# Optimization experiments

Measured on AMD Instinct MI355X. Metric: run time of the kernel, lower is better.

## Reference

```python
import jax, jax.numpy as jnp
import numpy as np
import math

D_MODEL = 1024
N_HEADS = 16
SPARSITY = 0.3


def setup_inputs() -> dict:
    key = jax.random.key(0)
    ks = jax.random.split(key, 12)
    B, S, D = 4, 2048, D_MODEL
    Dh = D // 2
    sc = 0.02
    inp = {
        "x": jax.random.normal(ks[0], (B, S, D), dtype=jnp.float32),
        "wq": jax.random.normal(ks[1], (D, D), dtype=jnp.float32) * sc,
        "bq": jnp.zeros((D,), jnp.float32),
        "wk": jax.random.normal(ks[2], (D, D), dtype=jnp.float32) * sc,
        "bk": jnp.zeros((D,), jnp.float32),
        "wv": jax.random.normal(ks[3], (D, D), dtype=jnp.float32) * sc,
        "bv": jnp.zeros((D,), jnp.float32),
        "wo": jax.random.normal(ks[4], (D, D), dtype=jnp.float32) * sc,
        "bo": jnp.zeros((D,), jnp.float32),
        "wi1": jax.random.normal(ks[5], (Dh, D), dtype=jnp.float32) * sc,
        "bi1": jnp.zeros((Dh,), jnp.float32),
        "wi2": jax.random.normal(ks[6], (1, Dh), dtype=jnp.float32) * sc,
        "bi2": jnp.zeros((1,), jnp.float32),
    }
    return inp


def reference(x, wq, bq, wk, bk, wv, bv, wo, bo, wi1, bi1, wi2, bi2):
    B, S, D = x.shape
    H = N_HEADS
    hd = D // H
    k = max(1, int(S * SPARSITY))

    # projections (torch Linear: x @ W^T + b)
    Q = (x @ wq.T + bq).reshape(B, S, H, hd).transpose(0, 2, 1, 3)  # [B,H,S,hd]
    K = (x @ wk.T + bk).reshape(B, S, H, hd).transpose(0, 2, 1, 3)
    V = (x @ wv.T + bv).reshape(B, S, H, hd).transpose(0, 2, 1, 3)

    # learned indexer -> per-position importance [B,S]
    h = jnp.maximum(x @ wi1.T + bi1, 0.0)
    importance = (h @ wi2.T + bi2)[..., 0]

    _, top_idx = jax.lax.top_k(importance, k)  # [B,k]
    sparse_mask = jnp.zeros((B, S), dtype=x.dtype).at[
        jnp.arange(B)[:, None], top_idx
    ].set(1.0)

    scores = jnp.einsum("bhqd,bhkd->bhqk", Q, K) / math.sqrt(hd)
    scores = jnp.where(sparse_mask[:, None, None, :] == 0, -jnp.inf, scores)
    attn = jax.nn.softmax(scores, axis=-1)

    out = jnp.einsum("bhqk,bhkd->bhqd", attn, V)
    out = out.transpose(0, 2, 1, 3).reshape(B, S, D)
    return out @ wo.T + bo
```

## Files before the change

kernel.cpp:

```cpp
#include <hip/hip_runtime.h>
#include <math.h>

#define BB 4
#define SS 2048
#define DD 1024
#define HHD 16
#define HD 64
#define DH 512
#define KSEL 614
#define KPAD 640
#define MTOT (BB*SS)
#define NCH (KPAD/64)
#define MKV (BB*KPAD)

typedef __attribute__((ext_vector_type(8))) short bf16x8;
typedef __attribute__((ext_vector_type(4))) float f32x4;

#define LDS_CAST(p) ((__attribute__((address_space(3))) void*)(p))
#define GLB_CAST(p) ((const __attribute__((address_space(1))) void*)(p))

#define QK_SCALE 0.18033688011112042f

__device__ inline short bf16rne(float v)
{
    unsigned u = __builtin_bit_cast(unsigned, v);
    return (short)((u + 0x7FFFu + ((u >> 16) & 1u)) >> 16);
}

__device__ inline void split1(float v, short& h, short& l)
{
    unsigned u = __builtin_bit_cast(unsigned, v);
    unsigned hr = (u + 0x7FFFu + ((u >> 16) & 1u)) >> 16;
    h = (short)hr;
    float hf = __builtin_bit_cast(float, hr << 16);
    float res = v - hf;
    unsigned u2 = __builtin_bit_cast(unsigned, res);
    unsigned lr = (u2 + 0x7FFFu + ((u2 >> 16) & 1u)) >> 16;
    l = (short)lr;
}

__global__ __launch_bounds__(256)
void split_convert(const float* __restrict__ in, short* __restrict__ hi,
                   short* __restrict__ lo, int n4)
{
    const int i = blockIdx.x * 256 + threadIdx.x;
    if (i >= n4) return;
    float4 v = reinterpret_cast<const float4*>(in)[i];
    short4 h, l;
    split1(v.x, h.x, l.x);
    split1(v.y, h.y, l.y);
    split1(v.z, h.z, l.z);
    split1(v.w, h.w, l.w);
    reinterpret_cast<short4*>(hi)[i] = h;
    reinterpret_cast<short4*>(lo)[i] = l;
}

__global__ __launch_bounds__(256)
void split_weights(const float* __restrict__ wq, const float* __restrict__ wk,
                   const float* __restrict__ wv, const float* __restrict__ wo,
                   const float* __restrict__ wi1,
                   const float* __restrict__ bk, const float* __restrict__ bv,
                   short* __restrict__ Bqkv_hi, short* __restrict__ wo_hi,
                   short* __restrict__ Wi_hi, short* __restrict__ Wi_lo,
                   float* __restrict__ bkv)
{
    const int i = blockIdx.x * 256 + threadIdx.x;
    const int which = blockIdx.y;
    if (which < 4) {
        const float* src = (which == 0) ? wq : (which == 1) ? wk : (which == 2) ? wv : wo;
        short* dst = (which == 3) ? wo_hi : (Bqkv_hi + (size_t)which * DD * DD);
        float4 v = reinterpret_cast<const float4*>(src)[i];
        short4 hh;
        hh.x = bf16rne(v.x); hh.y = bf16rne(v.y); hh.z = bf16rne(v.z); hh.w = bf16rne(v.w);
        reinterpret_cast<short4*>(dst)[i] = hh;
    } else if (which == 4) {
        if (i >= DH*DD/4) return;
        float4 v = reinterpret_cast<const float4*>(wi1)[i];
        short4 h, l;
        split1(v.x, h.x, l.x); split1(v.y, h.y, l.y);
        split1(v.z, h.z, l.z); split1(v.w, h.w, l.w);
        reinterpret_cast<short4*>(Wi_hi)[i] = h;
        reinterpret_cast<short4*>(Wi_lo)[i] = l;
    } else {
        if (i >= 2048) return;
        bkv[i] = (i < 1024) ? bk[i] : bv[i - 1024];
    }
}

template<bool BF16_OUT, bool QSCALE>
__global__ __launch_bounds__(256)
void gemm_bf16(const short* __restrict__ Ahi, const short* __restrict__ Bhi,
               const float* __restrict__ bias, void* __restrict__ Cv,
               int M, int N, int K, int ldc)
{
    __shared__ short sAh[128*64];
    __shared__ short sBh[128*64];

    const int t = threadIdx.x;
    const int lane = t & 63, wid = t >> 6;
    const int wm = wid >> 1, wn = wid & 1;
    const int row0 = blockIdx.y * 128, col0 = blockIdx.x * 128;
    const int g = lane >> 4, r = lane & 15;
    const int lrow = lane >> 3;
    const int lslot = lane & 7;

    f32x4 acc[4][4];
    #pragma unroll
    for (int mt = 0; mt < 4; ++mt)
        #pragma unroll
        for (int nt = 0; nt < 4; ++nt) acc[mt][nt] = (f32x4){0.f, 0.f, 0.f, 0.f};

    for (int k0 = 0; k0 < K; k0 += 64) {
        #pragma unroll
        for (int e = 0; e < 4; ++e) {
            const int rl = wid * 32 + e * 8 + lrow;
            const int scol = k0 + ((lslot ^ (rl & 7)) << 3);
            const size_t ga = (size_t)(row0 + rl) * K + scol;
            const size_t gb = (size_t)(col0 + rl) * K + scol;
            const int ldso = (wid * 32 + e * 8) * 64;
            __builtin_amdgcn_global_load_lds(GLB_CAST(Ahi + ga), LDS_CAST(sAh + ldso), 16, 0, 0);
            __builtin_amdgcn_global_load_lds(GLB_CAST(Bhi + gb), LDS_CAST(sBh + ldso), 16, 0, 0);
        }
        __syncthreads();

        #pragma unroll
        for (int kk = 0; kk < 2; ++kk) {
            bf16x8 ah[4], bh[4];
            #pragma unroll
            for (int mt = 0; mt < 4; ++mt) {
                const int rw = wm * 64 + mt * 16 + r;
                ah[mt] = *reinterpret_cast<const bf16x8*>(sAh + rw * 64 + (((kk*4 + g) ^ (rw & 7)) << 3));
            }
            #pragma unroll
            for (int nt = 0; nt < 4; ++nt) {
                const int rw = wn * 64 + nt * 16 + r;
                bh[nt] = *reinterpret_cast<const bf16x8*>(sBh + rw * 64 + (((kk*4 + g) ^ (rw & 7)) << 3));
            }
            #pragma unroll
            for (int mt = 0; mt < 4; ++mt)
                #pragma unroll
                for (int nt = 0; nt < 4; ++nt)
                    acc[mt][nt] = __builtin_amdgcn_mfma_f32_16x16x32_bf16(ah[mt], bh[nt], acc[mt][nt], 0, 0, 0);
        }
        __syncthreads();
    }

    #pragma unroll
    for (int nt = 0; nt < 4; ++nt) {
        const int col = wn * 64 + nt * 16 + r;
        const float bv = bias[col0 + col];
        const bool qs = QSCALE && (col0 + col) < 1024;
        #pragma unroll
        for (int mt = 0; mt < 4; ++mt) {
            #pragma unroll
            for (int e = 0; e < 4; ++e) {
                const int row = row0 + wm * 64 + mt * 16 + 4 * g + e;
                float v = acc[mt][nt][e] + bv;
                if (qs) v *= QK_SCALE;
                if (BF16_OUT)
                    ((short*)Cv)[(size_t)row * ldc + col0 + col] = bf16rne(v);
                else
                    ((float*)Cv)[(size_t)row * ldc + col0 + col] = v;
            }
        }
    }
}

__global__ __launch_bounds__(256)
void idx_q_fused(const short* __restrict__ x_hi, const short* __restrict__ x_lo,
                 const short* __restrict__ Wq_hi, const float* __restrict__ bq,
                 short* __restrict__ Qb,
                 const short* __restrict__ Wi_hi, const short* __restrict__ Wi_lo,
                 const float* __restrict__ bi1, float* __restrict__ Hw)
{
    __shared__ __align__(16) char smem[32768];
    const int t = threadIdx.x;
    const int lane = t & 63, wid = t >> 6;
    const int g = lane >> 4, r = lane & 15;

    if ((blockIdx.x & 1) == 0) {
        const int id = blockIdx.x >> 1;
        const int row0 = (id >> 3) * 128, col0 = (id & 7) * 128;
        short* sAh = (short*)smem;
        short* sBh = sAh + 128*64;
        const int wm = wid >> 1, wn = wid & 1;
        const int lrow = lane >> 3;
        const int lslot = lane & 7;

        f32x4 acc[4][4];
        #pragma unroll
        for (int mt = 0; mt < 4; ++mt)
            #pragma unroll
            for (int nt = 0; nt < 4; ++nt) acc[mt][nt] = (f32x4){0.f, 0.f, 0.f, 0.f};

        for (int k0 = 0; k0 < DD; k0 += 64) {
            #pragma unroll
            for (int e = 0; e < 4; ++e) {
                const int rl = wid * 32 + e * 8 + lrow;
                const int scol = k0 + ((lslot ^ (rl & 7)) << 3);
                const size_t ga = (size_t)(row0 + rl) * DD + scol;
                const size_t gb = (size_t)(col0 + rl) * DD + scol;
                const int ldso = (wid * 32 + e * 8) * 64;
                __builtin_amdgcn_global_load_lds(GLB_CAST(x_hi + ga), LDS_CAST(sAh + ldso), 16, 0, 0);
                __builtin_amdgcn_global_load_lds(GLB_CAST(Wq_hi + gb), LDS_CAST(sBh + ldso), 16, 0, 0);
            }
            __syncthreads();

            #pragma unroll
            for (int kk = 0; kk < 2; ++kk) {
                bf16x8 ah[4], bh[4];
                #pragma unroll
                for (int mt = 0; mt < 4; ++mt) {
                    const int rw = wm * 64 + mt * 16 + r;
                    ah[mt] = *reinterpret_cast<const bf16x8*>(sAh + rw * 64 + (((kk*4 + g) ^ (rw & 7)) << 3));
                }
                #pragma unroll
                for (int nt = 0; nt < 4; ++nt) {
                    const int rw = wn * 64 + nt * 16 + r;
                    bh[nt] = *reinterpret_cast<const bf16x8*>(sBh + rw * 64 + (((kk*4 + g) ^ (rw & 7)) << 3));
                }
                #pragma unroll
                for (int mt = 0; mt < 4; ++mt)
                    #pragma unroll
                    for (int nt = 0; nt < 4; ++nt)
                        acc[mt][nt] = __builtin_amdgcn_mfma_f32_16x16x32_bf16(ah[mt], bh[nt], acc[mt][nt], 0, 0, 0);
            }
            __syncthreads();
        }

        #pragma unroll
        for (int nt = 0; nt < 4; ++nt) {
            const int col = wn * 64 + nt * 16 + r;
            const float bv = bq[col0 + col];
            #pragma unroll
            for (int mt = 0; mt < 4; ++mt) {
                #pragma unroll
                for (int e = 0; e < 4; ++e) {
                    const int row = row0 + wm * 64 + mt * 16 + 4 * g + e;
                    Qb[(size_t)row * DD + col0 + col] = bf16rne((acc[mt][nt][e] + bv) * QK_SCALE);
                }
            }
        }
    } else {
        const int id = blockIdx.x >> 1;
        const int row0 = (id >> 2) * 64, col0 = (id & 3) * 128;
        short* sAh = (short*)smem;
        short* sAl = sAh + 64*32;
        short* sBh = sAl + 64*32;
        short* sBl = sBh + 128*32;
        const int srow = lane >> 2;
        const int sslot = lane & 3;

        f32x4 acc[4][2];
        #pragma unroll
        for (int mt = 0; mt < 4; ++mt)
            #pragma unroll
            for (int nt = 0; nt < 2; ++nt) acc[mt][nt] = (f32x4){0.f, 0.f, 0.f, 0.f};

        for (int k0 = 0; k0 < DD; k0 += 32) {
            {
                const int rl = wid * 16 + srow;
                const int scol = k0 + ((sslot ^ ((rl >> 2) & 3)) << 3);
                const size_t ga = (size_t)(row0 + rl) * DD + scol;
                const int ldso = (wid * 16) * 32;
                __builtin_amdgcn_global_load_lds(GLB_CAST(x_hi + ga), LDS_CAST(sAh + ldso), 16, 0, 0);
                __builtin_amdgcn_global_load_lds(GLB_CAST(x_lo + ga), LDS_CAST(sAl + ldso), 16, 0, 0);
            }
            #pragma unroll
            for (int i = 0; i < 2; ++i) {
                const int rl = i * 64 + wid * 16 + srow;
                const int scol = k0 + ((sslot ^ ((rl >> 2) & 3)) << 3);
                const size_t gb = (size_t)(col0 + rl) * DD + scol;
                const int ldso = (i * 64 + wid * 16) * 32;
                __builtin_amdgcn_global_load_lds(GLB_CAST(Wi_hi + gb), LDS_CAST(sBh + ldso), 16, 0, 0);
                __builtin_amdgcn_global_load_lds(GLB_CAST(Wi_lo + gb), LDS_CAST(sBl + ldso), 16, 0, 0);
            }
            __syncthreads();

            bf16x8 ah[4], al[4], bh[2], bl[2];
            #pragma unroll
            for (int mt = 0; mt < 4; ++mt) {
                const int row = mt * 16 + r;
                const int sw = g ^ ((row >> 2) & 3);
                ah[mt] = *reinterpret_cast<const bf16x8*>(sAh + row * 32 + sw * 8);
                al[mt] = *reinterpret_cast<const bf16x8*>(sAl + row * 32 + sw * 8);
            }
            #pragma unroll
            for (int nt = 0; nt < 2; ++nt) {
                const int row = wid * 32 + nt * 16 + r;
                const int sw = g ^ ((row >> 2) & 3);
                bh[nt] = *reinterpret_cast<const bf16x8*>(sBh + row * 32 + sw * 8);
                bl[nt] = *reinterpret_cast<const bf16x8*>(sBl + row * 32 + sw * 8);
            }
            #pragma unroll
            for (int mt = 0; mt < 4; ++mt)
                #pragma unroll
                for (int nt = 0; nt < 2; ++nt) {
                    acc[mt][nt] = __builtin_amdgcn_mfma_f32_16x16x32_bf16(ah[mt], bh[nt], acc[mt][nt], 0, 0, 0);
                    acc[mt][nt] = __builtin_amdgcn_mfma_f32_16x16x32_bf16(ah[mt], bl[nt], acc[mt][nt], 0, 0, 0);
                    acc[mt][nt] = __builtin_amdgcn_mfma_f32_16x16x32_bf16(al[mt], bh[nt], acc[mt][nt], 0, 0, 0);
                }
            __syncthreads();
        }

        #pragma unroll
        for (int nt = 0; nt < 2; ++nt) {
            const int col = wid * 32 + nt * 16 + r;
            const float bv = bi1[col0 + col];
            #pragma unroll
            for (int mt = 0; mt < 4; ++mt) {
                #pragma unroll
                for (int e = 0; e < 4; ++e) {
                    const int row = row0 + mt * 16 + 4 * g + e;
                    Hw[(size_t)row * DH + col0 + col] = fmaxf(acc[mt][nt][e] + bv, 0.f);
                }
            }
        }
    }
}

__global__ __launch_bounds__(256)
void gemm_kv_gather(const short* __restrict__ Ahi, const short* __restrict__ Bhi,
                    const int* __restrict__ idxg, const float* __restrict__ bias,
                    short* __restrict__ C)
{
    __shared__ short sAh[128*64];
    __shared__ short sBh[128*64];

    const int K = DD, N = 2048;
    const int t = threadIdx.x;
    const int lane = t & 63, wid = t >> 6;
    const int wm = wid >> 1, wn = wid & 1;
    const int row0 = blockIdx.y * 128, col0 = blockIdx.x * 128;
    const int g = lane >> 4, r = lane & 15;
    const int lrow = lane >> 3;
    const int lslot = lane & 7;

    size_t garow[4];
    #pragma unroll
    for (int e = 0; e < 4; ++e) {
        const int rl = row0 + wid * 32 + e * 8 + lrow;
        const int grow = (rl / KPAD) * SS + idxg[rl];
        garow[e] = (size_t)grow * K;
    }

    f32x4 acc[4][4];
    #pragma unroll
    for (int mt = 0; mt < 4; ++mt)
        #pragma unroll
        for (int nt = 0; nt < 4; ++nt) acc[mt][nt] = (f32x4){0.f, 0.f, 0.f, 0.f};

    for (int k0 = 0; k0 < K; k0 += 64) {
        #pragma unroll
        for (int e = 0; e < 4; ++e) {
            const int rl = wid * 32 + e * 8 + lrow;
            const int scol = k0 + ((lslot ^ (rl & 7)) << 3);
            const size_t gb = (size_t)(col0 + rl) * K + scol;
            const int ldso = (wid * 32 + e * 8) * 64;
            __builtin_amdgcn_global_load_lds(GLB_CAST(Ahi + garow[e] + scol), LDS_CAST(sAh + ldso), 16, 0, 0);
            __builtin_amdgcn_global_load_lds(GLB_CAST(Bhi + gb), LDS_CAST(sBh + ldso), 16, 0, 0);
        }
        __syncthreads();

        #pragma unroll
        for (int kk = 0; kk < 2; ++kk) {
            bf16x8 ah[4], bh[4];
            #pragma unroll
            for (int mt = 0; mt < 4; ++mt) {
                const int rw = wm * 64 + mt * 16 + r;
                ah[mt] = *reinterpret_cast<const bf16x8*>(sAh + rw * 64 + (((kk*4 + g) ^ (rw & 7)) << 3));
            }
            #pragma unroll
            for (int nt = 0; nt < 4; ++nt) {
                const int rw = wn * 64 + nt * 16 + r;
                bh[nt] = *reinterpret_cast<const bf16x8*>(sBh + rw * 64 + (((kk*4 + g) ^ (rw & 7)) << 3));
            }
            #pragma unroll
            for (int mt = 0; mt < 4; ++mt)
                #pragma unroll
                for (int nt = 0; nt < 4; ++nt)
                    acc[mt][nt] = __builtin_amdgcn_mfma_f32_16x16x32_bf16(ah[mt], bh[nt], acc[mt][nt], 0, 0, 0);
        }
        __syncthreads();
    }

    #pragma unroll
    for (int nt = 0; nt < 4; ++nt) {
        const int col = wn * 64 + nt * 16 + r;
        const float bv = bias[col0 + col];
        #pragma unroll
        for (int mt = 0; mt < 4; ++mt) {
            #pragma unroll
            for (int e = 0; e < 4; ++e) {
                const int row = row0 + wm * 64 + mt * 16 + 4 * g + e;
                C[(size_t)row * N + col0 + col] = bf16rne(acc[mt][nt][e] + bv);
            }
        }
    }
}

__global__ __launch_bounds__(256)
void importance_kernel(const float* __restrict__ h, const float* __restrict__ wi2,
                       const float* __restrict__ bi2, float* __restrict__ imp)
{
    const int wid = threadIdx.x >> 6, lane = threadIdx.x & 63;
    const int row = blockIdx.x * 4 + wid;
    const float* hr = h + (size_t)row * DH;
    float s = 0.f;
    #pragma unroll
    for (int i = 0; i < DH/64; ++i)
        s = fmaf(hr[lane + i*64], wi2[lane + i*64], s);
    #pragma unroll
    for (int off = 32; off; off >>= 1) s += __shfl_down(s, off);
    if (lane == 0) imp[row] = s + bi2[0];
}

__global__ __launch_bounds__(256)
void rank_kernel(const float* __restrict__ imp, int* __restrict__ flags)
{
    __shared__ float simp[SS];
    const int b = blockIdx.y;
    const int t = threadIdx.x;
    const float* bimp = imp + b * SS;
    for (int i = t; i < SS/4; i += 256)
        reinterpret_cast<float4*>(simp)[i] = reinterpret_cast<const float4*>(bimp)[i];
    __syncthreads();

    const int i = blockIdx.x * 32 + (t >> 3);
    const int part = t & 7;
    const float v = simp[i];
    const float4* slice = reinterpret_cast<const float4*>(simp + part * (SS/8));
    const int jb = part * (SS/8);
    int rank = 0;
    #pragma unroll 8
    for (int jj = 0; jj < SS/32; ++jj) {
        const float4 u4 = slice[jj];
        const int j = jb + jj * 4;
        rank += (u4.x > v) || ((u4.x == v) && (j + 0 < i));
        rank += (u4.y > v) || ((u4.y == v) && (j + 1 < i));
        rank += (u4.z > v) || ((u4.z == v) && (j + 2 < i));
        rank += (u4.w > v) || ((u4.w == v) && (j + 3 < i));
    }
    rank += __shfl_xor(rank, 1);
    rank += __shfl_xor(rank, 2);
    rank += __shfl_xor(rank, 4);
    if (part == 0) flags[b * SS + i] = (rank < KSEL) ? 1 : 0;
}

__global__ __launch_bounds__(256)
void compact_kernel(const int* __restrict__ flags, int* __restrict__ idxg)
{
    __shared__ int sscan[SS];
    __shared__ int sidx[KSEL];
    const int b = blockIdx.x, t = threadIdx.x;
    for (int i = t; i < SS; i += 256) sscan[i] = flags[b * SS + i];
    __syncthreads();
    for (int off = 1; off < SS; off <<= 1) {
        int vals[SS/256];
        #pragma unroll
        for (int c = 0; c < SS/256; ++c) {
            const int i = t + c * 256;
            int v = sscan[i];
            if (i >= off) v += sscan[i - off];
            vals[c] = v;
        }
        __syncthreads();
        #pragma unroll
        for (int c = 0; c < SS/256; ++c) sscan[t + c * 256] = vals[c];
        __syncthreads();
    }
    for (int i = t; i < SS; i += 256) {
        const int f = flags[b * SS + i];
        if (f) sidx[sscan[i] - 1] = i;
    }
    __syncthreads();
    for (int p = t; p < KPAD; p += 256)
        idxg[b * KPAD + p] = sidx[min(p, KSEL - 1)];
}

__global__ __launch_bounds__(256)
void gather_kv(const short* __restrict__ KVc, short* __restrict__ Kg,
               short* __restrict__ Vg)
{
    __shared__ short Vs[64*72];
    const int t = threadIdx.x;
    const int c = blockIdx.x, h = blockIdx.y, b = blockIdx.z;
    const int srow = t >> 2;
    const int sq4  = t & 3;

    const size_t cbase = ((size_t)(b * HHD + h) * NCH + c) * 4096;

    const short* kb = KVc + (size_t)(b * KPAD + c * 64 + srow) * 2048 + h * HD + sq4 * 16;
    bf16x8 k0 = *reinterpret_cast<const bf16x8*>(kb);
    bf16x8 k1 = *reinterpret_cast<const bf16x8*>(kb + 8);
    short* kout = Kg + cbase + srow * HD + sq4 * 16;
    *reinterpret_cast<bf16x8*>(kout)     = k0;
    *reinterpret_cast<bf16x8*>(kout + 8) = k1;

    const short* vbp = kb + 1024;
    bf16x8 v0 = *reinterpret_cast<const bf16x8*>(vbp);
    bf16x8 v1 = *reinterpret_cast<const bf16x8*>(vbp + 8);
    #pragma unroll
    for (int j = 0; j < 8; ++j) {
        Vs[(sq4 * 16 + j) * 72 + srow]     = v0[j];
        Vs[(sq4 * 16 + 8 + j) * 72 + srow] = v1[j];
    }
    __syncthreads();

    const int x = 8 * (srow >> 4);
    short* vout = Vg + cbase + srow * 64;
    *reinterpret_cast<bf16x8*>(vout + ((sq4 * 16)     ^ x)) = *reinterpret_cast<const bf16x8*>(&Vs[srow * 72 + sq4 * 16]);
    *reinterpret_cast<bf16x8*>(vout + ((sq4 * 16 + 8) ^ x)) = *reinterpret_cast<const bf16x8*>(&Vs[srow * 72 + sq4 * 16 + 8]);
}

__global__ __launch_bounds__(512)
void attn_mfma(const short* __restrict__ Qb, const short* __restrict__ Kg,
               const short* __restrict__ Vg, short* __restrict__ AOhi)
{
    __shared__ short Ks[2][64*72];
    __shared__ short Vs[2][64*72];
    __shared__ short Ps[8][16*72];

    const int t = threadIdx.x;
    const int lane = t & 63, w = t >> 6;
    const int g = lane >> 4, r = lane & 15;
    const int qt = blockIdx.x, h = blockIdx.y, b = blockIdx.z;
    const int q0 = qt * 128;
    short* Psw = &Ps[w][0];

    const int srow = t >> 3;
    const int scol = (t & 7) * 8;
    const short* kcbase = Kg + ((size_t)(b * HHD + h) * NCH) * 4096 + srow * 64 + scol;
    const short* vcbase = Vg + ((size_t)(b * HHD + h) * NCH) * 4096 + srow * 64 + scol;

    bf16x8 qh[2];
    {
        const short* qrow = Qb + (size_t)(b * SS + q0 + w * 16 + r) * DD + h * HD;
        qh[0] = *reinterpret_cast<const bf16x8*>(qrow + 8 * g);
        qh[1] = *reinterpret_cast<const bf16x8*>(qrow + 32 + 8 * g);
    }

    bf16x8 ones;
    #pragma unroll
    for (int j = 0; j < 8; ++j) ones[j] = (short)0x3F80;

    f32x4 oacc[4];
    #pragma unroll
    for (int dt = 0; dt < 4; ++dt) oacc[dt] = (f32x4){0.f, 0.f, 0.f, 0.f};
    f32x4 dacc = (f32x4){0.f, 0.f, 0.f, 0.f};

    bf16x8 kreg = *reinterpret_cast<const bf16x8*>(kcbase);
    bf16x8 vreg = *reinterpret_cast<const bf16x8*>(vcbase);

    for (int c = 0; c < NCH; ++c) {
        const int cur = c & 1;
        *reinterpret_cast<bf16x8*>(&Ks[cur][srow*72 + scol]) = kreg;
        *reinterpret_cast<bf16x8*>(&Vs[cur][srow*72 + scol]) = vreg;
        if (c + 1 < NCH) {
            kreg = *reinterpret_cast<const bf16x8*>(kcbase + (size_t)(c + 1) * 4096);
            vreg = *reinterpret_cast<const bf16x8*>(vcbase + (size_t)(c + 1) * 4096);
        }
        __syncthreads();

        f32x4 sa[4];
        #pragma unroll
        for (int kt = 0; kt < 4; ++kt) {
            bf16x8 kf0 = *reinterpret_cast<const bf16x8*>(&Ks[cur][(kt*16 + r)*72 + 8*g]);
            bf16x8 kf1 = *reinterpret_cast<const bf16x8*>(&Ks[cur][(kt*16 + r)*72 + 32 + 8*g]);
            f32x4 s = (f32x4){0.f, 0.f, 0.f, 0.f};
            s = __builtin_amdgcn_mfma_f32_16x16x32_bf16(qh[0], kf0, s, 0, 0, 0);
            s = __builtin_amdgcn_mfma_f32_16x16x32_bf16(qh[1], kf1, s, 0, 0, 0);
            sa[kt] = s;
        }
        if (c == NCH - 1) {
            #pragma unroll
            for (int kt = 0; kt < 4; ++kt)
                if (c*64 + kt*16 + r >= KSEL)
                    sa[kt] = (f32x4){-INFINITY, -INFINITY, -INFINITY, -INFINITY};
        }

        #pragma unroll
        for (int kt = 0; kt < 4; ++kt)
            #pragma unroll
            for (int e = 0; e < 4; ++e)
                Psw[(4*g + e)*72 + ((kt*16 + r) ^ (8*g))] =
                    (short)(__builtin_bit_cast(unsigned, exp2f(sa[kt][e])) >> 16);

        #pragma unroll
        for (int kc = 0; kc < 2; ++kc) {
            bf16x8 pf = *reinterpret_cast<const bf16x8*>(&Psw[r*72 + kc*32 + 8*(g ^ (r >> 2))]);
            dacc = __builtin_amdgcn_mfma_f32_16x16x32_bf16(pf, ones, dacc, 0, 0, 0);
            #pragma unroll
            for (int dt = 0; dt < 4; ++dt) {
                bf16x8 vf = *reinterpret_cast<const bf16x8*>(&Vs[cur][(dt*16 + r)*72 + kc*32 + 8*(g ^ dt)]);
                oacc[dt] = __builtin_amdgcn_mfma_f32_16x16x32_bf16(pf, vf, oacc[dt], 0, 0, 0);
            }
        }
    }

    #pragma unroll
    for (int dt = 0; dt < 4; ++dt)
        #pragma unroll
        for (int e = 0; e < 4; ++e) {
            const size_t a = (size_t)(b * SS + q0 + w*16 + 4*g + e) * DD + h * HD + dt*16 + r;
            AOhi[a] = bf16rne(oacc[dt][e] / dacc[e]);
        }
}

extern "C" void kernel_launch(void* const* d_in, const int* in_sizes, int n_in,
                              void* d_out, int out_size, void* d_ws, size_t ws_size,
                              hipStream_t stream)
{
    const float* x   = (const float*)d_in[0];
    const float* wq  = (const float*)d_in[1];
    const float* bq  = (const float*)d_in[2];
    const float* wk  = (const float*)d_in[3];
    const float* bk  = (const float*)d_in[4];
    const float* wv  = (const float*)d_in[5];
    const float* bv  = (const float*)d_in[6];
    const float* wo  = (const float*)d_in[7];
    const float* bo  = (const float*)d_in[8];
    const float* wi1 = (const float*)d_in[9];
    const float* bi1 = (const float*)d_in[10];
    const float* wi2 = (const float*)d_in[11];
    const float* bi2 = (const float*)d_in[12];
    float* out = (float*)d_out;

    const size_t MB = 1ull << 20;
    char* W = (char*)d_ws;
    short* x_hi  = (short*)(W + 0);
    short* x_lo  = (short*)(W + 16*MB);
    short* Qb    = (short*)(W + 32*MB);
    short* KVc   = (short*)(W + 48*MB);
    short* Wi_hi = (short*)(W + 96*MB);
    short* Wi_lo = (short*)(W + 97*MB);
    short* Bqkv_hi=(short*)(W + 128*MB);
    short* wo_hi = (short*)(W + 134*MB);
    float* Hw    = (float*)(W + 144*MB);
    short* Kg    = (short*)(W + 144*MB);
    short* Vg    = (short*)(W + 150*MB);
    float* bkv   = (float*)(W + 160*MB);
    float* imp   = (float*)(W + 160*MB + 64*1024);
    int*   flags = (int*)(W + 160*MB + 128*1024);
    int*   idxg  = (int*)(W + 160*MB + 192*1024);
    short* AO_hi = x_hi;

    const size_t NM = (size_t)MTOT * DD;

    split_convert<<<(NM/4 + 255)/256, 256, 0, stream>>>(x, x_hi, x_lo, NM/4);
    split_weights<<<dim3(DD*DD/4/256, 6), 256, 0, stream>>>(
        wq, wk, wv, wo, wi1, bk, bv, Bqkv_hi, wo_hi, Wi_hi, Wi_lo, bkv);

    idx_q_fused<<<1024, 256, 0, stream>>>(
        x_hi, x_lo, Bqkv_hi, bq, Qb, Wi_hi, Wi_lo, bi1, Hw);

    importance_kernel<<<MTOT/4, 256, 0, stream>>>(Hw, wi2, bi2, imp);
    rank_kernel<<<dim3(SS/32, BB), 256, 0, stream>>>(imp, flags);
    compact_kernel<<<BB, 256, 0, stream>>>(flags, idxg);

    gemm_kv_gather<<<dim3(2048/128, MKV/128), 256, 0, stream>>>(
        x_hi, Bqkv_hi + (size_t)DD*DD, idxg, bkv, KVc);

    gather_kv<<<dim3(NCH, HHD, BB), 256, 0, stream>>>(KVc, Kg, Vg);

    attn_mfma<<<dim3(SS/128, HHD, BB), 512, 0, stream>>>(Qb, Kg, Vg, AO_hi);

    gemm_bf16<false, false><<<dim3(DD/128, MTOT/128), 256, 0, stream>>>(
        AO_hi, wo_hi, bo, out, MTOT, DD, DD, DD);
}
```

Baseline: 200.4 us.

## Fuse Q and gathered KV projections into one kernel, scatter KV directly

```diff
diff --git a/kernel.cpp b/kernel.cpp
--- a/kernel.cpp
+++ b/kernel.cpp
@@ -87,10 +87,9 @@
     }
 }
 
-template<bool BF16_OUT, bool QSCALE>
 __global__ __launch_bounds__(256)
 void gemm_bf16(const short* __restrict__ Ahi, const short* __restrict__ Bhi,
-               const float* __restrict__ bias, void* __restrict__ Cv,
+               const float* __restrict__ bias, float* __restrict__ C,
                int M, int N, int K, int ldc)
 {
     __shared__ short sAh[128*64];
@@ -149,49 +148,43 @@
     for (int nt = 0; nt < 4; ++nt) {
         const int col = wn * 64 + nt * 16 + r;
         const float bv = bias[col0 + col];
-        const bool qs = QSCALE && (col0 + col) < 1024;
         #pragma unroll
         for (int mt = 0; mt < 4; ++mt) {
             #pragma unroll
             for (int e = 0; e < 4; ++e) {
                 const int row = row0 + wm * 64 + mt * 16 + 4 * g + e;
-                float v = acc[mt][nt][e] + bv;
-                if (qs) v *= QK_SCALE;
-                if (BF16_OUT)
-                    ((short*)Cv)[(size_t)row * ldc + col0 + col] = bf16rne(v);
-                else
-                    ((float*)Cv)[(size_t)row * ldc + col0 + col] = v;
-            }
-        }
-    }
-}
-
-__global__ __launch_bounds__(256)
-void idx_q_fused(const short* __restrict__ x_hi, const short* __restrict__ x_lo,
-                 const short* __restrict__ Wq_hi, const float* __restrict__ bq,
-                 short* __restrict__ Qb,
-                 const short* __restrict__ Wi_hi, const short* __restrict__ Wi_lo,
-                 const float* __restrict__ bi1, float* __restrict__ Hw)
+                C[(size_t)row * ldc + col0 + col] = acc[mt][nt][e] + bv;
+            }
+        }
+    }
+}
+
+__global__ __launch_bounds__(256)
+void qkv_fused(const short* __restrict__ x_hi, const short* __restrict__ Bqkv_hi,
+               const float* __restrict__ bq, const float* __restrict__ bkv,
+               const int* __restrict__ idxg,
+               short* __restrict__ Qb, short* __restrict__ Kg, short* __restrict__ Vg)
 {
     __shared__ __align__(16) char smem[32768];
+    short* sAh = (short*)smem;
+    short* sBh = sAh + 128*64;
+
     const int t = threadIdx.x;
     const int lane = t & 63, wid = t >> 6;
+    const int wm = wid >> 1, wn = wid & 1;
     const int g = lane >> 4, r = lane & 15;
-
-    if ((blockIdx.x & 1) == 0) {
-        const int id = blockIdx.x >> 1;
+    const int lrow = lane >> 3;
+    const int lslot = lane & 7;
+
+    f32x4 acc[4][4];
+    #pragma unroll
+    for (int mt = 0; mt < 4; ++mt)
+        #pragma unroll
+        for (int nt = 0; nt < 4; ++nt) acc[mt][nt] = (f32x4){0.f, 0.f, 0.f, 0.f};
+
+    if (blockIdx.x < 512) {
+        const int id = blockIdx.x;
         const int row0 = (id >> 3) * 128, col0 = (id & 7) * 128;
-        short* sAh = (short*)smem;
-        short* sBh = sAh + 128*64;
-        const int wm = wid >> 1, wn = wid & 1;
-        const int lrow = lane >> 3;
-        const int lslot = lane & 7;
-
-        f32x4 acc[4][4];
-        #pragma unroll
-        for (int mt = 0; mt < 4; ++mt)
-            #pragma unroll
-            for (int nt = 0; nt < 4; ++nt) acc[mt][nt] = (f32x4){0.f, 0.f, 0.f, 0.f};
 
         for (int k0 = 0; k0 < DD; k0 += 64) {
             #pragma unroll
@@ -202,7 +195,7 @@
                 const size_t gb = (size_t)(col0 + rl) * DD + scol;
                 const int ldso = (wid * 32 + e * 8) * 64;
                 __builtin_amdgcn_global_load_lds(GLB_CAST(x_hi + ga), LDS_CAST(sAh + ldso), 16, 0, 0);
-                __builtin_amdgcn_global_load_lds(GLB_CAST(Wq_hi + gb), LDS_CAST(sBh + ldso), 16, 0, 0);
+                __builtin_amdgcn_global_load_lds(GLB_CAST(Bqkv_hi + gb), LDS_CAST(sBh + ldso), 16, 0, 0);
             }
             __syncthreads();
 
@@ -242,158 +235,163 @@
             }
         }
     } else {
-        const int id = blockIdx.x >> 1;
-        const int row0 = (id >> 2) * 64, col0 = (id & 3) * 128;
-        short* sAh = (short*)smem;
-        short* sAl = sAh + 64*32;
-        short* sBh = sAl + 64*32;
-        short* sBl = sBh + 128*32;
-        const int srow = lane >> 2;
-        const int sslot = lane & 3;
-
-        f32x4 acc[4][2];
-        #pragma unroll
-        for (int mt = 0; mt < 4; ++mt)
-            #pragma unroll
-            for (int nt = 0; nt < 2; ++nt) acc[mt][nt] = (f32x4){0.f, 0.f, 0.f, 0.f};
-
-        for (int k0 = 0; k0 < DD; k0 += 32) {
-            {
-                const int rl = wid * 16 + srow;
-                const int scol = k0 + ((sslot ^ ((rl >> 2) & 3)) << 3);
-                const size_t ga = (size_t)(row0 + rl) * DD + scol;
-                const int ldso = (wid * 16) * 32;
-                __builtin_amdgcn_global_load_lds(GLB_CAST(x_hi + ga), LDS_CAST(sAh + ldso), 16, 0, 0);
-                __builtin_amdgcn_global_load_lds(GLB_CAST(x_lo + ga), LDS_CAST(sAl + ldso), 16, 0, 0);
-            }
-            #pragma unroll
-            for (int i = 0; i < 2; ++i) {
-                const int rl = i * 64 + wid * 16 + srow;
-                const int scol = k0 + ((sslot ^ ((rl >> 2) & 3)) << 3);
+        const int id = blockIdx.x - 512;
+        const int row0 = (id >> 4) * 128;
+        const int col0 = (id & 15) * 128;
+        const short* Bw = Bqkv_hi + (size_t)DD * DD;
+
+        size_t garow[4];
+        #pragma unroll
+        for (int e = 0; e < 4; ++e) {
+            const int rl = row0 + wid * 32 + e * 8 + lrow;
+            const int grow = (rl / KPAD) * SS + idxg[rl];
+            garow[e] = (size_t)grow * DD;
+        }
+
+        for (int k0 = 0; k0 < DD; k0 += 64) {
+            #pragma unroll
+            for (int e = 0; e < 4; ++e) {
+                const int rl = wid * 32 + e * 8 + lrow;
+                const int scol = k0 + ((lslot ^ (rl & 7)) << 3);
                 const size_t gb = (size_t)(col0 + rl) * DD + scol;
-                const int ldso = (i * 64 + wid * 16) * 32;
-                __builtin_amdgcn_global_load_lds(GLB_CAST(Wi_hi + gb), LDS_CAST(sBh + ldso), 16, 0, 0);
-                __builtin_amdgcn_global_load_lds(GLB_CAST(Wi_lo + gb), LDS_CAST(sBl + ldso), 16, 0, 0);
+                const int ldso = (wid * 32 + e * 8) * 64;
+                __builtin_amdgcn_global_load_lds(GLB_CAST(x_hi + garow[e] + scol), LDS_CAST(sAh + ldso), 16, 0, 0);
+                __builtin_amdgcn_global_load_lds(GLB_CAST(Bw + gb), LDS_CAST(sBh + ldso), 16, 0, 0);
             }
             __syncthreads();
 
-            bf16x8 ah[4], al[4], bh[2], bl[2];
+            #pragma unroll
+            for (int kk = 0; kk < 2; ++kk) {
+                bf16x8 ah[4], bh[4];
+                #pragma unroll
+                for (int mt = 0; mt < 4; ++mt) {
+                    const int rw = wm * 64 + mt * 16 + r;
+                    ah[mt] = *reinterpret_cast<const bf16x8*>(sAh + rw * 64 + (((kk*4 + g) ^ (rw & 7)) << 3));
+                }
+                #pragma unroll
+                for (int nt = 0; nt < 4; ++nt) {
+                    const int rw = wn * 64 + nt * 16 + r;
+                    bh[nt] = *reinterpret_cast<const bf16x8*>(sBh + rw * 64 + (((kk*4 + g) ^ (rw & 7)) << 3));
+                }
+                #pragma unroll
+                for (int mt = 0; mt < 4; ++mt)
+                    #pragma unroll
+                    for (int nt = 0; nt < 4; ++nt)
+                        acc[mt][nt] = __builtin_amdgcn_mfma_f32_16x16x32_bf16(ah[mt], bh[nt], acc[mt][nt], 0, 0, 0);
+            }
+            __syncthreads();
+        }
+
+        #pragma unroll
+        for (int nt = 0; nt < 4; ++nt) {
+            const int col = col0 + wn * 64 + nt * 16 + r;
+            const float bv = bkv[col];
+            const bool isK = col < 1024;
+            const int cc = isK ? col : (col - 1024);
+            const int h = cc >> 6, d = cc & 63;
             #pragma unroll
             for (int mt = 0; mt < 4; ++mt) {
-                const int row = mt * 16 + r;
-                const int sw = g ^ ((row >> 2) & 3);
-                ah[mt] = *reinterpret_cast<const bf16x8*>(sAh + row * 32 + sw * 8);
-                al[mt] = *reinterpret_cast<const bf16x8*>(sAl + row * 32 + sw * 8);
-            }
-            #pragma unroll
-            for (int nt = 0; nt < 2; ++nt) {
-                const int row = wid * 32 + nt * 16 + r;
-                const int sw = g ^ ((row >> 2) & 3);
-                bh[nt] = *reinterpret_cast<const bf16x8*>(sBh + row * 32 + sw * 8);
-                bl[nt] = *reinterpret_cast<const bf16x8*>(sBl + row * 32 + sw * 8);
-            }
-            #pragma unroll
-            for (int mt = 0; mt < 4; ++mt)
-                #pragma unroll
-                for (int nt = 0; nt < 2; ++nt) {
-                    acc[mt][nt] = __builtin_amdgcn_mfma_f32_16x16x32_bf16(ah[mt], bh[nt], acc[mt][nt], 0, 0, 0);
-                    acc[mt][nt] = __builtin_amdgcn_mfma_f32_16x16x32_bf16(ah[mt], bl[nt], acc[mt][nt], 0, 0, 0);
-                    acc[mt][nt] = __builtin_amdgcn_mfma_f32_16x16x32_bf16(al[mt], bh[nt], acc[mt][nt], 0, 0, 0);
+                #pragma unroll
+                for (int e = 0; e < 4; ++e) {
+                    const int kvrow = row0 + wm * 64 + mt * 16 + 4 * g + e;
+                    const int b = kvrow / KPAD;
+                    const int rem = kvrow - b * KPAD;
+                    const int c = rem >> 6, key = rem & 63;
+                    const size_t cbase = ((size_t)(b * HHD + h) * NCH + c) * 4096;
+                    const short val = bf16rne(acc[mt][nt][e] + bv);
+                    if (isK)
+                        Kg[cbase + key * 64 + d] = val;
+                    else
+                        Vg[cbase + d * 64 + (key ^ (8 * (d >> 4)))] = val;
                 }
-            __syncthreads();
-        }
-
-        #pragma unroll
-        for (int nt = 0; nt < 2; ++nt) {
-            const int col = wid * 32 + nt * 16 + r;
-            const float bv = bi1[col0 + col];
-            #pragma unroll
-            for (int mt = 0; mt < 4; ++mt) {
-                #pragma unroll
-                for (int e = 0; e < 4; ++e) {
-                    const int row = row0 + mt * 16 + 4 * g + e;
-                    Hw[(size_t)row * DH + col0 + col] = fmaxf(acc[mt][nt][e] + bv, 0.f);
-                }
-            }
-        }
-    }
-}
-
-__global__ __launch_bounds__(256)
-void gemm_kv_gather(const short* __restrict__ Ahi, const short* __restrict__ Bhi,
-                    const int* __restrict__ idxg, const float* __restrict__ bias,
-                    short* __restrict__ C)
-{
-    __shared__ short sAh[128*64];
-    __shared__ short sBh[128*64];
-
-    const int K = DD, N = 2048;
+            }
+        }
+    }
+}
+
+template<bool RELU>
+__global__ __launch_bounds__(256)
+void gemm_split64(const short* __restrict__ Ahi, const short* __restrict__ Alo,
+                  const short* __restrict__ Bhi, const short* __restrict__ Blo,
+                  const float* __restrict__ bias, float* __restrict__ C,
+                  int M, int N, int K, int ldc)
+{
+    __shared__ short sAh[64*32];
+    __shared__ short sAl[64*32];
+    __shared__ short sBh[128*32];
+    __shared__ short sBl[128*32];
+
     const int t = threadIdx.x;
     const int lane = t & 63, wid = t >> 6;
-    const int wm = wid >> 1, wn = wid & 1;
-    const int row0 = blockIdx.y * 128, col0 = blockIdx.x * 128;
+    const int row0 = blockIdx.y * 64, col0 = blockIdx.x * 128;
     const int g = lane >> 4, r = lane & 15;
-    const int lrow = lane >> 3;
-    const int lslot = lane & 7;
-
-    size_t garow[4];
-    #pragma unroll
-    for (int e = 0; e < 4; ++e) {
-        const int rl = row0 + wid * 32 + e * 8 + lrow;
-        const int grow = (rl / KPAD) * SS + idxg[rl];
-        garow[e] = (size_t)grow * K;
-    }
-
-    f32x4 acc[4][4];
+    const int srow = lane >> 2;
+    const int sslot = lane & 3;
+
+    f32x4 acc[4][2];
     #pragma unroll
     for (int mt = 0; mt < 4; ++mt)
         #pragma unroll
-        for (int nt = 0; nt < 4; ++nt) acc[mt][nt] = (f32x4){0.f, 0.f, 0.f, 0.f};
-
-    for (int k0 = 0; k0 < K; k0 += 64) {
-        #pragma unroll
-        for (int e = 0; e < 4; ++e) {
-            const int rl = wid * 32 + e * 8 + lrow;
-            const int scol = k0 + ((lslot ^ (rl & 7)) << 3);
+        for (int nt = 0; nt < 2; ++nt) acc[mt][nt] = (f32x4){0.f, 0.f, 0.f, 0.f};
+
+    for (int k0 = 0; k0 < K; k0 += 32) {
+        {
+            const int rl = wid * 16 + srow;
+            const int scol = k0 + ((sslot ^ ((rl >> 2) & 3)) << 3);
+            const size_t ga = (size_t)(row0 + rl) * K + scol;
+            const int ldso = (wid * 16) * 32;
+            __builtin_amdgcn_global_load_lds(GLB_CAST(Ahi + ga), LDS_CAST(sAh + ldso), 16, 0, 0);
+            __builtin_amdgcn_global_load_lds(GLB_CAST(Alo + ga), LDS_CAST(sAl + ldso), 16, 0, 0);
+        }
+        #pragma unroll
+        for (int i = 0; i < 2; ++i) {
+            const int rl = i * 64 + wid * 16 + srow;
+            const int scol = k0 + ((sslot ^ ((rl >> 2) & 3)) << 3);
             const size_t gb = (size_t)(col0 + rl) * K + scol;
-            const int ldso = (wid * 32 + e * 8) * 64;
-            __builtin_amdgcn_global_load_lds(GLB_CAST(Ahi + garow[e] + scol), LDS_CAST(sAh + ldso), 16, 0, 0);
+            const int ldso = (i * 64 + wid * 16) * 32;
             __builtin_amdgcn_global_load_lds(GLB_CAST(Bhi + gb), LDS_CAST(sBh + ldso), 16, 0, 0);
+            __builtin_amdgcn_global_load_lds(GLB_CAST(Blo + gb), LDS_CAST(sBl + ldso), 16, 0, 0);
         }
         __syncthreads();
 
-        #pragma unroll
-        for (int kk = 0; kk < 2; ++kk) {
-            bf16x8 ah[4], bh[4];
-            #pragma unroll
-            for (int mt = 0; mt < 4; ++mt) {
-                const int rw = wm * 64 + mt * 16 + r;
-                ah[mt] = *reinterpret_cast<const bf16x8*>(sAh + rw * 64 + (((kk*4 + g) ^ (rw & 7)) << 3));
-            }
-            #pragma unroll
-            for (int nt = 0; nt < 4; ++nt) {
-                const int rw = wn * 64 + nt * 16 + r;
-                bh[nt] = *reinterpret_cast<const bf16x8*>(sBh + rw * 64 + (((kk*4 + g) ^ (rw & 7)) << 3));
-            }
-            #pragma unroll
-            for (int mt = 0; mt < 4; ++mt)
-                #pragma unroll
-                for (int nt = 0; nt < 4; ++nt)
-                    acc[mt][nt] = __builtin_amdgcn_mfma_f32_16x16x32_bf16(ah[mt], bh[nt], acc[mt][nt], 0, 0, 0);
-        }
+        bf16x8 ah[4], al[4], bh[2], bl[2];
+        #pragma unroll
+        for (int mt = 0; mt < 4; ++mt) {
+            const int row = mt * 16 + r;
+            const int sw = g ^ ((row >> 2) & 3);
+            ah[mt] = *reinterpret_cast<const bf16x8*>(sAh + row * 32 + sw * 8);
+            al[mt] = *reinterpret_cast<const bf16x8*>(sAl + row * 32 + sw * 8);
+        }
+        #pragma unroll
+        for (int nt = 0; nt < 2; ++nt) {
+            const int row = wid * 32 + nt * 16 + r;
+            const int sw = g ^ ((row >> 2) & 3);
+            bh[nt] = *reinterpret_cast<const bf16x8*>(sBh + row * 32 + sw * 8);
+            bl[nt] = *reinterpret_cast<const bf16x8*>(sBl + row * 32 + sw * 8);
+        }
+        #pragma unroll
+        for (int mt = 0; mt < 4; ++mt)
+            #pragma unroll
+            for (int nt = 0; nt < 2; ++nt) {
+                acc[mt][nt] = __builtin_amdgcn_mfma_f32_16x16x32_bf16(ah[mt], bh[nt], acc[mt][nt], 0, 0, 0);
+                acc[mt][nt] = __builtin_amdgcn_mfma_f32_16x16x32_bf16(ah[mt], bl[nt], acc[mt][nt], 0, 0, 0);
+                acc[mt][nt] = __builtin_amdgcn_mfma_f32_16x16x32_bf16(al[mt], bh[nt], acc[mt][nt], 0, 0, 0);
+            }
         __syncthreads();
     }
 
     #pragma unroll
-    for (int nt = 0; nt < 4; ++nt) {
-        const int col = wn * 64 + nt * 16 + r;
+    for (int nt = 0; nt < 2; ++nt) {
+        const int col = wid * 32 + nt * 16 + r;
         const float bv = bias[col0 + col];
         #pragma unroll
         for (int mt = 0; mt < 4; ++mt) {
             #pragma unroll
             for (int e = 0; e < 4; ++e) {
-                const int row = row0 + wm * 64 + mt * 16 + 4 * g + e;
-                C[(size_t)row * N + col0 + col] = bf16rne(acc[mt][nt][e] + bv);
+                const int row = row0 + mt * 16 + 4 * g + e;
+                float v = acc[mt][nt][e] + bv;
+                if (RELU) v = fmaxf(v, 0.f);
+                C[(size_t)row * ldc + col0 + col] = v;
             }
         }
     }
@@ -478,41 +476,6 @@
         idxg[b * KPAD + p] = sidx[min(p, KSEL - 1)];
 }
 
-__global__ __launch_bounds__(256)
-void gather_kv(const short* __restrict__ KVc, short* __restrict__ Kg,
-               short* __restrict__ Vg)
-{
-    __shared__ short Vs[64*72];
-    const int t = threadIdx.x;
-    const int c = blockIdx.x, h = blockIdx.y, b = blockIdx.z;
-    const int srow = t >> 2;
-    const int sq4  = t & 3;
-
-    const size_t cbase = ((size_t)(b * HHD + h) * NCH + c) * 4096;
-
-    const short* kb = KVc + (size_t)(b * KPAD + c * 64 + srow) * 2048 + h * HD + sq4 * 16;
-    bf16x8 k0 = *reinterpret_cast<const bf16x8*>(kb);
-    bf16x8 k1 = *reinterpret_cast<const bf16x8*>(kb + 8);
-    short* kout = Kg + cbase + srow * HD + sq4 * 16;
-    *reinterpret_cast<bf16x8*>(kout)     = k0;
-    *reinterpret_cast<bf16x8*>(kout + 8) = k1;
-
-    const short* vbp = kb + 1024;
-    bf16x8 v0 = *reinterpret_cast<const bf16x8*>(vbp);
-    bf16x8 v1 = *reinterpret_cast<const bf16x8*>(vbp + 8);
-    #pragma unroll
-    for (int j = 0; j < 8; ++j) {
-        Vs[(sq4 * 16 + j) * 72 + srow]     = v0[j];
-        Vs[(sq4 * 16 + 8 + j) * 72 + srow] = v1[j];
-    }
-    __syncthreads();
-
-    const int x = 8 * (srow >> 4);
-    short* vout = Vg + cbase + srow * 64;
-    *reinterpret_cast<bf16x8*>(vout + ((sq4 * 16)     ^ x)) = *reinterpret_cast<const bf16x8*>(&Vs[srow * 72 + sq4 * 16]);
-    *reinterpret_cast<bf16x8*>(vout + ((sq4 * 16 + 8) ^ x)) = *reinterpret_cast<const bf16x8*>(&Vs[srow * 72 + sq4 * 16 + 8]);
-}
-
 __global__ __launch_bounds__(512)
 void attn_mfma(const short* __restrict__ Qb, const short* __restrict__ Kg,
                const short* __restrict__ Vg, short* __restrict__ AOhi)
@@ -631,7 +594,6 @@
     short* x_hi  = (short*)(W + 0);
     short* x_lo  = (short*)(W + 16*MB);
     short* Qb    = (short*)(W + 32*MB);
-    short* KVc   = (short*)(W + 48*MB);
     short* Wi_hi = (short*)(W + 96*MB);
     short* Wi_lo = (short*)(W + 97*MB);
     short* Bqkv_hi=(short*)(W + 128*MB);
@@ -651,20 +613,17 @@
     split_weights<<<dim3(DD*DD/4/256, 6), 256, 0, stream>>>(
         wq, wk, wv, wo, wi1, bk, bv, Bqkv_hi, wo_hi, Wi_hi, Wi_lo, bkv);
 
-    idx_q_fused<<<1024, 256, 0, stream>>>(
-        x_hi, x_lo, Bqkv_hi, bq, Qb, Wi_hi, Wi_lo, bi1, Hw);
-
+    gemm_split64<true><<<dim3(DH/128, MTOT/64), 256, 0, stream>>>(
+        x_hi, x_lo, Wi_hi, Wi_lo, bi1, Hw, MTOT, DH, DD, DH);
     importance_kernel<<<MTOT/4, 256, 0, stream>>>(Hw, wi2, bi2, imp);
     rank_kernel<<<dim3(SS/32, BB), 256, 0, stream>>>(imp, flags);
     compact_kernel<<<BB, 256, 0, stream>>>(flags, idxg);
 
-    gemm_kv_gather<<<dim3(2048/128, MKV/128), 256, 0, stream>>>(
-        x_hi, Bqkv_hi + (size_t)DD*DD, idxg, bkv, KVc);
-
-    gather_kv<<<dim3(NCH, HHD, BB), 256, 0, stream>>>(KVc, Kg, Vg);
+    qkv_fused<<<832, 256, 0, stream>>>(
+        x_hi, Bqkv_hi, bq, bkv, idxg, Qb, Kg, Vg);
 
     attn_mfma<<<dim3(SS/128, HHD, BB), 512, 0, stream>>>(Qb, Kg, Vg, AO_hi);
 
-    gemm_bf16<false, false><<<dim3(DD/128, MTOT/128), 256, 0, stream>>>(
+    gemm_bf16<<<dim3(DD/128, MTOT/128), 256, 0, stream>>>(
         AO_hi, wo_hi, bo, out, MTOT, DD, DD, DD);
 }
```

New measurement: 201.1 us. About the same (+0.3%).
